# Kernel optimization log

Measured on AMD Instinct MI355X. Metric: run time of the kernel, lower is better.

## Reference

```python
import jax, jax.numpy as jnp
import numpy as np
from jax import lax

NUM_HEADS = 1
DN = ('NCHW', 'OIHW', 'NCHW')
EPS = 1e-12  # F.normalize default eps


def _l2_normalize(t):
    # F.normalize(t, dim=-1): t / max(||t||_2, eps)
    n = jnp.sqrt(jnp.sum(t * t, axis=-1, keepdims=True))
    return t / jnp.maximum(n, EPS)


def setup_inputs() -> dict:
    key = jax.random.key(0)
    k0, k1, k2, k3 = jax.random.split(key, 4)
    b, c, h, w = 4, 48, 256, 256
    x = jax.random.normal(k0, (b, c, h, w), dtype=jnp.float32)
    qkv_w = jax.random.normal(k1, (3 * c, c, 1, 1), dtype=jnp.float32) * 0.05
    dw_w = jax.random.normal(k2, (3 * c, 1, 3, 3), dtype=jnp.float32) * 0.05
    proj_w = jax.random.normal(k3, (c, c, 1, 1), dtype=jnp.float32) * 0.05
    temperature = jnp.ones((NUM_HEADS, 1, 1), dtype=jnp.float32)
    return {"x": x, "qkv_w": qkv_w, "dw_w": dw_w, "proj_w": proj_w,
            "temperature": temperature}


def reference(x, qkv_w, dw_w, proj_w, temperature):
    b, c, h, w = x.shape
    heads = NUM_HEADS
    # 1x1 conv to 3c channels, then 3x3 depthwise conv (groups = 3c)
    qkv = lax.conv_general_dilated(x, qkv_w, (1, 1), 'VALID', dimension_numbers=DN)
    qkv = lax.conv_general_dilated(qkv, dw_w, (1, 1), ((1, 1), (1, 1)),
                                   feature_group_count=3 * c, dimension_numbers=DN)
    q, k, v = jnp.split(qkv, 3, axis=1)
    # [b, heads, c_per_head, h*w]
    q = q.reshape(b, heads, c // heads, h * w)
    k = k.reshape(b, heads, c // heads, h * w)
    v = v.reshape(b, heads, c // heads, h * w)
    q = _l2_normalize(q)
    k = _l2_normalize(k)
    # channel-wise attention: [b, heads, c_per_head, c_per_head]
    attn = jax.nn.softmax(jnp.einsum('bhcn,bhdn->bhcd', q, k) * temperature, axis=-1)
    out = jnp.einsum('bhcd,bhdn->bhcn', attn, v).reshape(b, c, h, w)
    return lax.conv_general_dilated(out, proj_w, (1, 1), 'VALID', dimension_numbers=DN)
```

## Files before the change

### kernel.cpp

```cpp
#include <hip/hip_runtime.h>

#define B 4
#define C 48
#define C3 144
#define H 256
#define W 256
#define HW 65536
#define EPSN 1e-12f

#define TSX 16
#define TSY 12
#define HSX 18
#define HSY 14
#define NTX 16
#define NTY 22
#define NPIX2 192
#define NHALO 252

#define NCHUNK 128
#define CHUNK 512
#define LP 68

#define S_QKV_OFF  ((size_t)0)
#define S_DWQ_OFF  (S_QKV_OFF + (size_t)B * C3 * HW)
#define S_DWK_OFF  (S_DWQ_OFF + (size_t)B * C * HW)
#define S_SP_OFF   (S_DWK_OFF + (size_t)B * C * HW)
#define S_NQP_OFF  (S_SP_OFF + (size_t)B * NCHUNK * C * C)
#define S_NKP_OFF  (S_NQP_OFF + (size_t)B * NCHUNK * C)
#define S_S_OFF    (S_NKP_OFF + (size_t)B * NCHUNK * C)
#define S_NQ_OFF   (S_S_OFF + (size_t)B * C * C)
#define S_NK_OFF   (S_NQ_OFF + (size_t)B * C)
#define S_M_OFF    (S_NK_OFF + (size_t)B * C)
#define S_WT_OFF   (S_M_OFF + (size_t)B * C * C)
#define S_FLOATS   (S_WT_OFF + (size_t)C3 * C)

#define A_DWQ_OFF  ((size_t)0)
#define A_DWK_OFF  (A_DWQ_OFF + (size_t)B * C * HW)
#define A_SP_OFF   (A_DWK_OFF + (size_t)B * C * HW)
#define A_NQP_OFF  (A_SP_OFF + (size_t)B * NCHUNK * C * C)
#define A_NKP_OFF  (A_NQP_OFF + (size_t)B * NCHUNK * C)
#define A_S_OFF    (A_NKP_OFF + (size_t)B * NCHUNK * C)
#define A_NQ_OFF   (A_S_OFF + (size_t)B * C * C)
#define A_NK_OFF   (A_NQ_OFF + (size_t)B * C)
#define A_M_OFF    (A_NK_OFF + (size_t)B * C)
#define A_FLOATS   (A_M_OFF + (size_t)B * C * C)

#define B_S_OFF  0
#define B_NQ_OFF (B * C * C)
#define B_NK_OFF (B_NQ_OFF + B * C)
#define B_M_OFF  (B_NK_OFF + B * C)
#define B_ZERO_N (B * C * C + 2 * B * C)


__global__ __launch_bounds__(256) void s_wt(
    const float* __restrict__ w1, float* __restrict__ wT) {
  const int i = blockIdx.x * 256 + threadIdx.x;
  if (i < C3 * C) {
    const int oc = i / C, d = i - oc * C;
    wT[d * C3 + oc] = w1[i];
  }
}

__global__ __launch_bounds__(256) void s_conv1x1(
    const float* __restrict__ x, const float* __restrict__ wT,
    float* __restrict__ qkv) {
  __shared__ float xs[C * 128];
  const int t = threadIdx.x;
  const int bb = blockIdx.x >> 9;
  const int p0 = (blockIdx.x & 511) << 7;
  const float* xb = x + (size_t)bb * C * HW + p0;
#pragma unroll
  for (int j = 0; j < 6; ++j) {
    const int f = t + j * 256;
    const int d = f >> 5, p4 = (f & 31) * 4;
    *(float4*)&xs[d * 128 + p4] = *(const float4*)&xb[(size_t)d * HW + p4];
  }
  __syncthreads();
  const int pl = (t & 63) * 2;
  const int ocw = __builtin_amdgcn_readfirstlane((t >> 6) * 12);
#pragma unroll 1
  for (int g = 0; g < 3; ++g) {
    const int oc0 = g * 48 + ocw;
    const float* wp = wT + oc0;
    float acc[12][2];
#pragma unroll
    for (int o = 0; o < 12; ++o)
#pragma unroll
      for (int p = 0; p < 2; ++p) acc[o][p] = 0.f;
#pragma unroll 4
    for (int d = 0; d < C; ++d) {
      const float2 xv = *(const float2*)&xs[d * 128 + pl];
      const float xa[2] = {xv.x, xv.y};
#pragma unroll
      for (int jj = 0; jj < 3; ++jj) {
        const float4 wv = *(const float4*)&wp[d * C3 + jj * 4];
        const float wa[4] = {wv.x, wv.y, wv.z, wv.w};
#pragma unroll
        for (int o = 0; o < 4; ++o)
#pragma unroll
          for (int p = 0; p < 2; ++p)
            acc[jj * 4 + o][p] = fmaf(wa[o], xa[p], acc[jj * 4 + o][p]);
      }
    }
    float* ob = qkv + ((size_t)bb * C3 + oc0) * HW + p0 + pl;
#pragma unroll
    for (int o = 0; o < 12; ++o) {
      float2 v;
      v.x = acc[o][0]; v.y = acc[o][1];
      *(float2*)&ob[(size_t)o * HW] = v;
    }
  }
}

#define DWR 16
__global__ __launch_bounds__(256) void s_dw(
    const float* __restrict__ qkv, const float* __restrict__ w9,
    float* __restrict__ dwq, float* __restrict__ dwk,
    float* __restrict__ vout) {
  __shared__ float ls[18 * 260];
  const int t = threadIdx.x;
  const int rblk = blockIdx.x & 15;
  const int cb = blockIdx.x >> 4;
  const int c = cb % C3;
  const int bb = cb / C3;
  const int r0 = rblk * DWR;
  const float* src = qkv + (size_t)cb * HW;
#pragma unroll
  for (int f = t; f < 18 * 256; f += 256) {
    const int rr = f >> 8, xc = f & 255;
    const int gr = r0 - 1 + rr;
    ls[rr * 260 + 1 + xc] = (gr >= 0 && gr < H) ? src[gr * W + xc] : 0.f;
  }
  if (t < 18) { ls[t * 260] = 0.f; ls[t * 260 + 257] = 0.f; }
  const float* wp = w9 + c * 9;
  float wv[9];
#pragma unroll
  for (int k = 0; k < 9; ++k) wv[k] = wp[k];
  __syncthreads();
  float* dst;
  int cc;
  if (c < C)          { dst = dwq;  cc = c; }
  else if (c < 2 * C) { dst = dwk;  cc = c - C; }
  else                { dst = vout; cc = c - 2 * C; }
  float* ob = dst + ((size_t)bb * C + cc) * HW;
  const int xq = (t & 63) * 4;
  const int rw = t >> 6;
#pragma unroll
  for (int rr = rw; rr < DWR; rr += 4) {
    const float* l0 = ls + rr * 260 + xq;
    const float4 a0 = *(const float4*)&l0[0];
    const float2 b0 = *(const float2*)&l0[4];
    const float4 a1 = *(const float4*)&l0[260];
    const float2 b1 = *(const float2*)&l0[264];
    const float4 a2 = *(const float4*)&l0[520];
    const float2 b2 = *(const float2*)&l0[524];
    const float r0e[6] = {a0.x, a0.y, a0.z, a0.w, b0.x, b0.y};
    const float r1e[6] = {a1.x, a1.y, a1.z, a1.w, b1.x, b1.y};
    const float r2e[6] = {a2.x, a2.y, a2.z, a2.w, b2.x, b2.y};
    float4 o;
    float* op = &o.x;
#pragma unroll
    for (int j = 0; j < 4; ++j) {
      float d = wv[0] * r0e[j] + wv[1] * r0e[j + 1] + wv[2] * r0e[j + 2];
      d = fmaf(wv[3], r1e[j], d);
      d = fmaf(wv[4], r1e[j + 1], d);
      d = fmaf(wv[5], r1e[j + 2], d);
      d = fmaf(wv[6], r2e[j], d);
      d = fmaf(wv[7], r2e[j + 1], d);
      d = fmaf(wv[8], r2e[j + 2], d);
      op[j] = d;
    }
    *(float4*)&ob[(r0 + rr) * W + xq] = o;
  }
}


__global__ __launch_bounds__(256) void a1_conv_dw(
    const float* __restrict__ x, const float* __restrict__ w1,
    const float* __restrict__ w9, float* __restrict__ dwq,
    float* __restrict__ dwk, float* __restrict__ vout) {
  __shared__ float xs[C * 256];
  __shared__ float qs[8 * 256];
  __shared__ float wg[C * 8];
  __shared__ float wg9[8 * 9];
  const int t = threadIdx.x;
  const int bb = blockIdx.x / (NTX * NTY);
  const int tile = blockIdx.x % (NTX * NTY);
  const int ty = tile / NTX, tx = tile % NTX;
  const int hyy = t / HSX, hxx = t % HSX;
  const int hy = ty * TSY - 1 + hyy;
  const int hx = tx * TSX - 1 + hxx;
  const bool hin = (t < NHALO) && (hy >= 0) && (hy < H) && (hx >= 0) && (hx < W);
  const float* xb = x + (size_t)bb * C * HW + (hin ? (hy * W + hx) : 0);
#pragma unroll
  for (int ic = 0; ic < C; ++ic)
    xs[ic * 256 + t] = hin ? xb[(size_t)ic * HW] : 0.f;
  const int py = t / TSX, px = t % TSX;
  const int gy = ty * TSY + py, gx = tx * TSX + px;
  const bool pin = (t < NPIX2) && (gy < H);
  const int hpos = py * HSX + px;
  for (int grp = 0; grp < 18; ++grp) {
    const int ch0 = grp * 8;
    {
      const int j = t + ((t < 128) ? 256 : 0);
      if (t < 128) {
        const int ic = t >> 3, g = t & 7;
        wg[t] = w1[(ch0 + g) * C + ic];
        const int ic2 = j >> 3, g2 = j & 7;
        wg[j] = w1[(ch0 + g2) * C + ic2];
      } else if (t < 256) {
        const int r = t - 128;
        const int ic = (r + 128) >> 3, g = (r + 128) & 7;
        wg[r + 128] = w1[(ch0 + g) * C + ic];
      }
      if (t < 72) wg9[t] = w9[ch0 * 9 + t];
    }
    __syncthreads();
    float a[8];
#pragma unroll
    for (int g = 0; g < 8; ++g) a[g] = 0.f;
#pragma unroll 4
    for (int ic = 0; ic < C; ++ic) {
      const float xsv = xs[ic * 256 + t];
      const float4 w0 = *(const float4*)&wg[ic * 8];
      const float4 w4 = *(const float4*)&wg[ic * 8 + 4];
      a[0] = fmaf(w0.x, xsv, a[0]);
      a[1] = fmaf(w0.y, xsv, a[1]);
      a[2] = fmaf(w0.z, xsv, a[2]);
      a[3] = fmaf(w0.w, xsv, a[3]);
      a[4] = fmaf(w4.x, xsv, a[4]);
      a[5] = fmaf(w4.y, xsv, a[5]);
      a[6] = fmaf(w4.z, xsv, a[6]);
      a[7] = fmaf(w4.w, xsv, a[7]);
    }
#pragma unroll
    for (int g = 0; g < 8; ++g) qs[g * 256 + t] = a[g];
    __syncthreads();
    if (t < NPIX2) {
#pragma unroll
      for (int g = 0; g < 8; ++g) {
        const int ch = ch0 + g;
        const float* w9p = wg9 + g * 9;
        const float* q = qs + g * 256 + hpos;
        float d = w9p[0] * q[0] + w9p[1] * q[1] + w9p[2] * q[2];
        d = fmaf(w9p[3], q[HSX], d);
        d = fmaf(w9p[4], q[HSX + 1], d);
        d = fmaf(w9p[5], q[HSX + 2], d);
        d = fmaf(w9p[6], q[2 * HSX], d);
        d = fmaf(w9p[7], q[2 * HSX + 1], d);
        d = fmaf(w9p[8], q[2 * HSX + 2], d);
        if (pin) {
          float* dst;
          int cc;
          if (ch < C)          { dst = dwq; cc = ch; }
          else if (ch < 2 * C) { dst = dwk; cc = ch - C; }
          else                 { dst = vout; cc = ch - 2 * C; }
          dst[((size_t)bb * C + cc) * HW + gy * W + gx] = d;
        }
      }
    }
    __syncthreads();
  }
}

__global__ __launch_bounds__(256) void a2_gram(
    const float* __restrict__ dwq, const float* __restrict__ dwk,
    float* __restrict__ Sp, float* __restrict__ nqp, float* __restrict__ nkp) {
  __shared__ float qs[C * LP];
  __shared__ float ks[C * LP];
  const int tid = threadIdx.x;
  const int bb = blockIdx.x / NCHUNK;
  const int chunk = blockIdx.x % NCHUNK;
  const int base = chunk * CHUNK;
  const float* qb = dwq + (size_t)bb * C * HW + base;
  const float* kb = dwk + (size_t)bb * C * HW + base;
  const int c0 = (tid >> 4) * 3;
  const int d0 = (tid & 15) * 3;
  float acc[3][3] = {{0.f}};
  float nacc = 0.f;
  float4 rq[3], rk[3];
#pragma unroll
  for (int j = 0; j < 3; ++j) {
    const int f = tid + j * 256;
    const int cc = f >> 4, p4 = (f & 15) * 4;
    rq[j] = *(const float4*)&qb[(size_t)cc * HW + p4];
    rk[j] = *(const float4*)&kb[(size_t)cc * HW + p4];
  }
  for (int sub = 0; sub < CHUNK / 64; ++sub) {
    __syncthreads();
#pragma unroll
    for (int j = 0; j < 3; ++j) {
      const int f = tid + j * 256;
      const int cc = f >> 4, p4 = (f & 15) * 4;
      *(float4*)&qs[cc * LP + p4] = rq[j];
      *(float4*)&ks[cc * LP + p4] = rk[j];
    }
    if (sub < CHUNK / 64 - 1) {
#pragma unroll
      for (int j = 0; j < 3; ++j) {
        const int f = tid + j * 256;
        const int cc = f >> 4, p4 = (f & 15) * 4;
        rq[j] = *(const float4*)&qb[(size_t)cc * HW + (sub + 1) * 64 + p4];
        rk[j] = *(const float4*)&kb[(size_t)cc * HW + (sub + 1) * 64 + p4];
      }
    }
    __syncthreads();
    if (tid < C) {
#pragma unroll
      for (int pq = 0; pq < 64; pq += 4) {
        const float4 v = *(const float4*)&qs[tid * LP + pq];
        nacc = fmaf(v.x, v.x, nacc);
        nacc = fmaf(v.y, v.y, nacc);
        nacc = fmaf(v.z, v.z, nacc);
        nacc = fmaf(v.w, v.w, nacc);
      }
    } else if (tid >= 64 && tid < 64 + C) {
      const int cq = tid - 64;
#pragma unroll
      for (int pq = 0; pq < 64; pq += 4) {
        const float4 v = *(const float4*)&ks[cq * LP + pq];
        nacc = fmaf(v.x, v.x, nacc);
        nacc = fmaf(v.y, v.y, nacc);
        nacc = fmaf(v.z, v.z, nacc);
        nacc = fmaf(v.w, v.w, nacc);
      }
    }
#pragma unroll 4
    for (int pq = 0; pq < 64; pq += 4) {
      const float4 q0 = *(const float4*)&qs[(c0 + 0) * LP + pq];
      const float4 q1 = *(const float4*)&qs[(c0 + 1) * LP + pq];
      const float4 q2 = *(const float4*)&qs[(c0 + 2) * LP + pq];
      const float4 k0 = *(const float4*)&ks[(d0 + 0) * LP + pq];
      const float4 k1 = *(const float4*)&ks[(d0 + 1) * LP + pq];
      const float4 k2 = *(const float4*)&ks[(d0 + 2) * LP + pq];
      const float qa[3][4] = {{q0.x, q0.y, q0.z, q0.w},
                              {q1.x, q1.y, q1.z, q1.w},
                              {q2.x, q2.y, q2.z, q2.w}};
      const float ka[3][4] = {{k0.x, k0.y, k0.z, k0.w},
                              {k1.x, k1.y, k1.z, k1.w},
                              {k2.x, k2.y, k2.z, k2.w}};
#pragma unroll
      for (int p = 0; p < 4; ++p)
#pragma unroll
        for (int i = 0; i < 3; ++i)
#pragma unroll
          for (int j = 0; j < 3; ++j)
            acc[i][j] = fmaf(qa[i][p], ka[j][p], acc[i][j]);
    }
  }
  float* Sb = Sp + ((size_t)bb * NCHUNK + chunk) * C * C;
#pragma unroll
  for (int i = 0; i < 3; ++i)
#pragma unroll
    for (int j = 0; j < 3; ++j)
      Sb[(c0 + i) * C + (d0 + j)] = acc[i][j];
  if (tid < C)                        nqp[((size_t)bb * NCHUNK + chunk) * C + tid] = nacc;
  else if (tid >= 64 && tid < 64 + C) nkp[((size_t)bb * NCHUNK + chunk) * C + (tid - 64)] = nacc;
}

#define RED_N (B * C * C + 2 * B * C)
__global__ __launch_bounds__(256) void a3a_reduce(
    const float* __restrict__ Sp, const float* __restrict__ nqp,
    const float* __restrict__ nkp, float* __restrict__ S,
    float* __restrict__ nq, float* __restrict__ nk) {
  const int gid = blockIdx.x * 256 + threadIdx.x;
  if (gid < B * C * C) {
    const int bb = gid / (C * C), j = gid - bb * (C * C);
    const float* src = Sp + (size_t)bb * NCHUNK * C * C + j;
    float s = 0.f;
#pragma unroll 8
    for (int i = 0; i < NCHUNK; ++i) s += src[(size_t)i * C * C];
    S[gid] = s;
  } else if (gid < B * C * C + B * C) {
    const int r = gid - B * C * C;
    const int bb = r / C, j = r - bb * C;
    const float* src = nqp + (size_t)bb * NCHUNK * C + j;
    float s = 0.f;
#pragma unroll 8
    for (int i = 0; i < NCHUNK; ++i) s += src[(size_t)i * C];
    nq[r] = s;
  } else if (gid < RED_N) {
    const int r = gid - B * C * C - B * C;
    const int bb = r / C, j = r - bb * C;
    const float* src = nkp + (size_t)bb * NCHUNK * C + j;
    float s = 0.f;
#pragma unroll 8
    for (int i = 0; i < NCHUNK; ++i) s += src[(size_t)i * C];
    nk[r] = s;
  }
}

__global__ __launch_bounds__(64) void a3b_attn(
    const float* __restrict__ S, const float* __restrict__ nq,
    const float* __restrict__ nk, const float* __restrict__ proj_w,
    const float* __restrict__ temperature, float* __restrict__ MT) {
  __shared__ float A[C * C];
  __shared__ float knl[C];
  const int bb = blockIdx.x;
  const int t = threadIdx.x;
  const float T = temperature[0];
  if (t < C) knl[t] = fmaxf(sqrtf(nk[bb * C + t]), EPSN);
  __syncthreads();
  if (t < C) {
    const float qn = fmaxf(sqrtf(nq[bb * C + t]), EPSN);
    float row[C];
    float m = -1e30f;
    for (int d = 0; d < C; ++d) {
      const float v = S[(size_t)bb * C * C + t * C + d] / (qn * knl[d]) * T;
      row[d] = v;
      m = fmaxf(m, v);
    }
    float sum = 0.f;
    for (int d = 0; d < C; ++d) { const float e = expf(row[d] - m); row[d] = e; sum += e; }
    const float inv = 1.f / sum;
    for (int d = 0; d < C; ++d) A[t * C + d] = row[d] * inv;
  }
  __syncthreads();
  for (int idx = t; idx < C * C; idx += 64) {
    const int e = idx / C, d = idx % C;
    float acc = 0.f;
    for (int cc = 0; cc < C; ++cc) acc = fmaf(proj_w[e * C + cc], A[cc * C + d], acc);
    MT[(size_t)bb * C * C + d * C + e] = acc;
  }
}

__global__ __launch_bounds__(256) void a4_apply(
    float* __restrict__ out, const float* __restrict__ MT) {
  __shared__ float vs[C * 128];
  const int t = threadIdx.x;
  const int bb = blockIdx.x >> 9;
  const int p0 = (blockIdx.x & 511) << 7;
  float* ob = out + (size_t)bb * C * HW + p0;
#pragma unroll
  for (int j = 0; j < 6; ++j) {
    const int f = t + j * 256;
    const int d = f >> 5, p4 = (f & 31) * 4;
    *(float4*)&vs[d * 128 + p4] = *(const float4*)&ob[(size_t)d * HW + p4];
  }
  __syncthreads();
  const int pl = (t & 63) * 2;
  const int e0 = __builtin_amdgcn_readfirstlane((t >> 6) * 12);
  const float* mb = MT + (size_t)bb * C * C + e0;
  float acc[12][2];
#pragma unroll
  for (int o = 0; o < 12; ++o)
#pragma unroll
    for (int p = 0; p < 2; ++p) acc[o][p] = 0.f;
#pragma unroll 4
  for (int d = 0; d < C; ++d) {
    const float2 xv = *(const float2*)&vs[d * 128 + pl];
    const float xa[2] = {xv.x, xv.y};
#pragma unroll
    for (int jj = 0; jj < 3; ++jj) {
      const float4 wv = *(const float4*)&mb[d * C + jj * 4];
      const float wa[4] = {wv.x, wv.y, wv.z, wv.w};
#pragma unroll
      for (int o = 0; o < 4; ++o)
#pragma unroll
        for (int p = 0; p < 2; ++p)
          acc[jj * 4 + o][p] = fmaf(wa[o], xa[p], acc[jj * 4 + o][p]);
    }
  }
#pragma unroll
  for (int o = 0; o < 12; ++o) {
    float2 v;
    v.x = acc[o][0]; v.y = acc[o][1];
    *(float2*)&ob[(size_t)(e0 + o) * HW + pl] = v;
  }
}


__global__ __launch_bounds__(256) void k0_zero(float* __restrict__ ws) {
  const int i = blockIdx.x * 256 + threadIdx.x;
  if (i < B_ZERO_N) ws[i] = 0.f;
}

#define TS 14
#define HS 16
#define NT 19
#define NPIX 196

__global__ __launch_bounds__(256) void k1_fused(
    const float* __restrict__ x, const float* __restrict__ w1,
    const float* __restrict__ w9, float* __restrict__ vout,
    float* __restrict__ S, float* __restrict__ nq, float* __restrict__ nk) {
  __shared__ float qs[4 * 256];
  __shared__ float qt[NPIX * C];
  __shared__ float kt[NPIX * C];
  const int t = threadIdx.x;
  const int bb = blockIdx.x / (NT * NT);
  const int tile = blockIdx.x % (NT * NT);
  const int ty = tile / NT, tx = tile % NT;
  const int hy = ty * TS - 1 + (t >> 4);
  const int hx = tx * TS - 1 + (t & 15);
  const bool hin = (hy >= 0 && hy < H && hx >= 0 && hx < W);
  const float* xb = x + (size_t)bb * C * HW;
  float xv[C];
#pragma unroll
  for (int ic = 0; ic < C; ++ic)
    xv[ic] = hin ? xb[(size_t)ic * HW + hy * W + hx] : 0.f;
  const int py = t / TS, px = t % TS;
  const int gy = ty * TS + py, gx = tx * TS + px;
  const bool pin = (t < NPIX) && (gy < H) && (gx < W);
  for (int grp = 0; grp < 36; ++grp) {
    const int ch0 = grp * 4;
    const float* wp = w1 + ch0 * C;
    float a0 = 0.f, a1 = 0.f, a2 = 0.f, a3 = 0.f;
#pragma unroll
    for (int ic = 0; ic < C; ++ic) {
      const float xs = xv[ic];
      a0 = fmaf(wp[ic], xs, a0);
      a1 = fmaf(wp[C + ic], xs, a1);
      a2 = fmaf(wp[2 * C + ic], xs, a2);
      a3 = fmaf(wp[3 * C + ic], xs, a3);
    }
    qs[0 * 256 + t] = a0;
    qs[1 * 256 + t] = a1;
    qs[2 * 256 + t] = a2;
    qs[3 * 256 + t] = a3;
    __syncthreads();
    if (t < NPIX) {
#pragma unroll
      for (int g = 0; g < 4; ++g) {
        const int ch = ch0 + g;
        const float* w9p = w9 + ch * 9;
        const float* q = qs + g * 256 + py * HS + px;
        float d = w9p[0] * q[0] + w9p[1] * q[1] + w9p[2] * q[2];
        d = fmaf(w9p[3], q[HS], d);
        d = fmaf(w9p[4], q[HS + 1], d);
        d = fmaf(w9p[5], q[HS + 2], d);
        d = fmaf(w9p[6], q[2 * HS], d);
        d = fmaf(w9p[7], q[2 * HS + 1], d);
        d = fmaf(w9p[8], q[2 * HS + 2], d);
        if (ch < C)          qt[t * C + ch] = pin ? d : 0.f;
        else if (ch < 2 * C) kt[t * C + (ch - C)] = pin ? d : 0.f;
        else if (pin)        vout[((size_t)bb * C + (ch - 2 * C)) * HW + gy * W + gx] = d;
      }
    }
    __syncthreads();
  }
  if (t < C) {
    float s = 0.f;
    for (int p = 0; p < NPIX; ++p) { const float v = qt[p * C + t]; s = fmaf(v, v, s); }
    atomicAdd(&nq[bb * C + t], s);
  } else if (t >= 64 && t < 64 + C) {
    const int c = t - 64;
    float s = 0.f;
    for (int p = 0; p < NPIX; ++p) { const float v = kt[p * C + c]; s = fmaf(v, v, s); }
    atomicAdd(&nk[bb * C + c], s);
  }
  {
    const int part = t >> 6;
    const int idx = t & 63;
    const int c0 = (idx >> 3) * 6;
    const int d0 = (idx & 7) * 6;
    float acc[6][6] = {{0.f}};
    const int p0 = part * 49;
    for (int p = p0; p < p0 + 49; ++p) {
      float qv[6], kv[6];
#pragma unroll
      for (int j = 0; j < 6; ++j) { qv[j] = qt[p * C + c0 + j]; kv[j] = kt[p * C + d0 + j]; }
#pragma unroll
      for (int i = 0; i < 6; ++i)
#pragma unroll
        for (int j = 0; j < 6; ++j) acc[i][j] = fmaf(qv[i], kv[j], acc[i][j]);
    }
    float* Sb = S + (size_t)bb * C * C;
#pragma unroll
    for (int i = 0; i < 6; ++i)
#pragma unroll
      for (int j = 0; j < 6; ++j) atomicAdd(&Sb[(c0 + i) * C + (d0 + j)], acc[i][j]);
  }
}


extern "C" void kernel_launch(void* const* d_in, const int* in_sizes, int n_in,
                              void* d_out, int out_size, void* d_ws, size_t ws_size,
                              hipStream_t stream) {
  const float* x      = (const float*)d_in[0];
  const float* qkv_w  = (const float*)d_in[1];
  const float* dw_w   = (const float*)d_in[2];
  const float* proj_w = (const float*)d_in[3];
  const float* temp   = (const float*)d_in[4];
  float* out = (float*)d_out;
  float* ws  = (float*)d_ws;

  if (ws_size >= S_FLOATS * sizeof(float)) {
    float* qkv = ws + S_QKV_OFF;
    float* dwq = ws + S_DWQ_OFF;
    float* dwk = ws + S_DWK_OFF;
    float* Sp  = ws + S_SP_OFF;
    float* nqp = ws + S_NQP_OFF;
    float* nkp = ws + S_NKP_OFF;
    float* S   = ws + S_S_OFF;
    float* nq  = ws + S_NQ_OFF;
    float* nk  = ws + S_NK_OFF;
    float* MT  = ws + S_M_OFF;
    float* wT  = ws + S_WT_OFF;
    s_wt<<<(C3 * C + 255) / 256, 256, 0, stream>>>(qkv_w, wT);
    s_conv1x1<<<B * 512, 256, 0, stream>>>(x, wT, qkv);
    s_dw<<<B * C3 * 16, 256, 0, stream>>>(qkv, dw_w, dwq, dwk, out);
    a2_gram<<<B * NCHUNK, 256, 0, stream>>>(dwq, dwk, Sp, nqp, nkp);
    a3a_reduce<<<(RED_N + 255) / 256, 256, 0, stream>>>(Sp, nqp, nkp, S, nq, nk);
    a3b_attn<<<B, 64, 0, stream>>>(S, nq, nk, proj_w, temp, MT);
    a4_apply<<<B * 512, 256, 0, stream>>>(out, MT);
  } else if (ws_size >= A_FLOATS * sizeof(float)) {
    float* dwq = ws + A_DWQ_OFF;
    float* dwk = ws + A_DWK_OFF;
    float* Sp  = ws + A_SP_OFF;
    float* nqp = ws + A_NQP_OFF;
    float* nkp = ws + A_NKP_OFF;
    float* S   = ws + A_S_OFF;
    float* nq  = ws + A_NQ_OFF;
    float* nk  = ws + A_NK_OFF;
    float* MT  = ws + A_M_OFF;
    a1_conv_dw<<<B * NTX * NTY, 256, 0, stream>>>(x, qkv_w, dw_w, dwq, dwk, out);
    a2_gram<<<B * NCHUNK, 256, 0, stream>>>(dwq, dwk, Sp, nqp, nkp);
    a3a_reduce<<<(RED_N + 255) / 256, 256, 0, stream>>>(Sp, nqp, nkp, S, nq, nk);
    a3b_attn<<<B, 64, 0, stream>>>(S, nq, nk, proj_w, temp, MT);
    a4_apply<<<B * 512, 256, 0, stream>>>(out, MT);
  } else {
    float* S  = ws + B_S_OFF;
    float* nq = ws + B_NQ_OFF;
    float* nk = ws + B_NK_OFF;
    float* MT = ws + B_M_OFF;
    k0_zero<<<(B_ZERO_N + 255) / 256, 256, 0, stream>>>(ws);
    k1_fused<<<B * NT * NT, 256, 0, stream>>>(x, qkv_w, dw_w, out, S, nq, nk);
    a3b_attn<<<B, 64, 0, stream>>>(S, nq, nk, proj_w, temp, MT);
    a4_apply<<<B * 512, 256, 0, stream>>>(out, MT);
  }
}
```

Baseline: 337.8 us.

## Fuse depthwise conv with Gram/norm partials, dropping dwq/dwk intermediates

Replaces the separate depthwise-conv kernel and Gram kernel in the large-workspace path with one kernel per image row. It computes the 3x3 depthwise conv for all 144 channels, keeps q/k in shared memory and accumulates the 48x48 Gram partials and squared norms directly. V is still written out to global memory. This removes the global write and re-read of the dwq/dwk tensors. In exchange, the conv now reads its stencil taps straight from global memory (relying on cache reuse) with one thread per pixel, and there are twice as many partial chunks for the reduce kernel to sum.

```diff
diff --git a/kernel.cpp b/kernel.cpp
--- a/kernel.cpp
+++ b/kernel.cpp
@@ -21,13 +21,14 @@
 #define CHUNK 512
 #define LP 68
 
+#define NCH2 256
+#define LP2 132
+
 #define S_QKV_OFF  ((size_t)0)
-#define S_DWQ_OFF  (S_QKV_OFF + (size_t)B * C3 * HW)
-#define S_DWK_OFF  (S_DWQ_OFF + (size_t)B * C * HW)
-#define S_SP_OFF   (S_DWK_OFF + (size_t)B * C * HW)
-#define S_NQP_OFF  (S_SP_OFF + (size_t)B * NCHUNK * C * C)
-#define S_NKP_OFF  (S_NQP_OFF + (size_t)B * NCHUNK * C)
-#define S_S_OFF    (S_NKP_OFF + (size_t)B * NCHUNK * C)
+#define S_SP_OFF   (S_QKV_OFF + (size_t)B * C3 * HW)
+#define S_NQP_OFF  (S_SP_OFF + (size_t)B * NCH2 * C * C)
+#define S_NKP_OFF  (S_NQP_OFF + (size_t)B * NCH2 * C)
+#define S_S_OFF    (S_NKP_OFF + (size_t)B * NCH2 * C)
 #define S_NQ_OFF   (S_S_OFF + (size_t)B * C * C)
 #define S_NK_OFF   (S_NQ_OFF + (size_t)B * C)
 #define S_M_OFF    (S_NK_OFF + (size_t)B * C)
@@ -112,66 +113,103 @@
   }
 }
 
-#define DWR 16
-__global__ __launch_bounds__(256) void s_dw(
+__global__ __launch_bounds__(256) void s_dwgram(
     const float* __restrict__ qkv, const float* __restrict__ w9,
-    float* __restrict__ dwq, float* __restrict__ dwk,
-    float* __restrict__ vout) {
-  __shared__ float ls[18 * 260];
+    float* __restrict__ vout, float* __restrict__ Sp,
+    float* __restrict__ nqp, float* __restrict__ nkp) {
+  __shared__ float qk[96 * LP2];
   const int t = threadIdx.x;
-  const int rblk = blockIdx.x & 15;
-  const int cb = blockIdx.x >> 4;
-  const int c = cb % C3;
-  const int bb = cb / C3;
-  const int r0 = rblk * DWR;
-  const float* src = qkv + (size_t)cb * HW;
-#pragma unroll
-  for (int f = t; f < 18 * 256; f += 256) {
-    const int rr = f >> 8, xc = f & 255;
-    const int gr = r0 - 1 + rr;
-    ls[rr * 260 + 1 + xc] = (gr >= 0 && gr < H) ? src[gr * W + xc] : 0.f;
-  }
-  if (t < 18) { ls[t * 260] = 0.f; ls[t * 260 + 257] = 0.f; }
-  const float* wp = w9 + c * 9;
-  float wv[9];
-#pragma unroll
-  for (int k = 0; k < 9; ++k) wv[k] = wp[k];
-  __syncthreads();
-  float* dst;
-  int cc;
-  if (c < C)          { dst = dwq;  cc = c; }
-  else if (c < 2 * C) { dst = dwk;  cc = c - C; }
-  else                { dst = vout; cc = c - 2 * C; }
-  float* ob = dst + ((size_t)bb * C + cc) * HW;
-  const int xq = (t & 63) * 4;
-  const int rw = t >> 6;
-#pragma unroll
-  for (int rr = rw; rr < DWR; rr += 4) {
-    const float* l0 = ls + rr * 260 + xq;
-    const float4 a0 = *(const float4*)&l0[0];
-    const float2 b0 = *(const float2*)&l0[4];
-    const float4 a1 = *(const float4*)&l0[260];
-    const float2 b1 = *(const float2*)&l0[264];
-    const float4 a2 = *(const float4*)&l0[520];
-    const float2 b2 = *(const float2*)&l0[524];
-    const float r0e[6] = {a0.x, a0.y, a0.z, a0.w, b0.x, b0.y};
-    const float r1e[6] = {a1.x, a1.y, a1.z, a1.w, b1.x, b1.y};
-    const float r2e[6] = {a2.x, a2.y, a2.z, a2.w, b2.x, b2.y};
-    float4 o;
-    float* op = &o.x;
-#pragma unroll
-    for (int j = 0; j < 4; ++j) {
-      float d = wv[0] * r0e[j] + wv[1] * r0e[j + 1] + wv[2] * r0e[j + 2];
-      d = fmaf(wv[3], r1e[j], d);
-      d = fmaf(wv[4], r1e[j + 1], d);
-      d = fmaf(wv[5], r1e[j + 2], d);
-      d = fmaf(wv[6], r2e[j], d);
-      d = fmaf(wv[7], r2e[j + 1], d);
-      d = fmaf(wv[8], r2e[j + 2], d);
-      op[j] = d;
-    }
-    *(float4*)&ob[(r0 + rr) * W + xq] = o;
-  }
+  const int bb = blockIdx.x >> 8;
+  const int y  = blockIdx.x & 255;
+  const float* qb = qkv + (size_t)bb * C3 * HW;
+  const int lx = t & 127;
+  const int chH = t >> 7;
+  const int c0 = (t >> 4) * 3;
+  const int d0 = (t & 15) * 3;
+  float acc[3][3] = {{0.f}};
+  float nacc = 0.f;
+#pragma unroll 1
+  for (int sub = 0; sub < 2; ++sub) {
+    const int x = sub * 128 + lx;
+    const bool okm = (x > 0);
+    const bool okp = (x < W - 1);
+    __syncthreads();
+#pragma unroll 2
+    for (int cp = 0; cp < 72; ++cp) {
+      const int ch = cp * 2 + chH;
+      const float* wp = w9 + ch * 9;
+      float wv[9];
+#pragma unroll
+      for (int k2 = 0; k2 < 9; ++k2) wv[k2] = wp[k2];
+      float s = 0.f;
+#pragma unroll
+      for (int dy = 0; dy < 3; ++dy) {
+        const int ry = y + dy - 1;
+        if (ry >= 0 && ry < H) {
+          const float* r = qb + (size_t)ch * HW + ry * W;
+          const float vm = okm ? r[x - 1] : 0.f;
+          const float vc = r[x];
+          const float vp = okp ? r[x + 1] : 0.f;
+          s = fmaf(wv[dy * 3 + 0], vm, s);
+          s = fmaf(wv[dy * 3 + 1], vc, s);
+          s = fmaf(wv[dy * 3 + 2], vp, s);
+        }
+      }
+      if (ch < 96) qk[ch * LP2 + lx] = s;
+      else vout[((size_t)bb * C + (ch - 96)) * HW + y * W + x] = s;
+    }
+    __syncthreads();
+    if (t < C) {
+#pragma unroll
+      for (int pq = 0; pq < 128; pq += 4) {
+        const float4 v = *(const float4*)&qk[t * LP2 + pq];
+        nacc = fmaf(v.x, v.x, nacc);
+        nacc = fmaf(v.y, v.y, nacc);
+        nacc = fmaf(v.z, v.z, nacc);
+        nacc = fmaf(v.w, v.w, nacc);
+      }
+    } else if (t >= 64 && t < 64 + C) {
+      const int cq = 48 + (t - 64);
+#pragma unroll
+      for (int pq = 0; pq < 128; pq += 4) {
+        const float4 v = *(const float4*)&qk[cq * LP2 + pq];
+        nacc = fmaf(v.x, v.x, nacc);
+        nacc = fmaf(v.y, v.y, nacc);
+        nacc = fmaf(v.z, v.z, nacc);
+        nacc = fmaf(v.w, v.w, nacc);
+      }
+    }
+#pragma unroll 4
+    for (int pq = 0; pq < 128; pq += 4) {
+      const float4 q0 = *(const float4*)&qk[(c0 + 0) * LP2 + pq];
+      const float4 q1 = *(const float4*)&qk[(c0 + 1) * LP2 + pq];
+      const float4 q2 = *(const float4*)&qk[(c0 + 2) * LP2 + pq];
+      const float4 k0 = *(const float4*)&qk[(48 + d0 + 0) * LP2 + pq];
+      const float4 k1 = *(const float4*)&qk[(48 + d0 + 1) * LP2 + pq];
+      const float4 k2 = *(const float4*)&qk[(48 + d0 + 2) * LP2 + pq];
+      const float qa[3][4] = {{q0.x, q0.y, q0.z, q0.w},
+                              {q1.x, q1.y, q1.z, q1.w},
+                              {q2.x, q2.y, q2.z, q2.w}};
+      const float ka[3][4] = {{k0.x, k0.y, k0.z, k0.w},
+                              {k1.x, k1.y, k1.z, k1.w},
+                              {k2.x, k2.y, k2.z, k2.w}};
+#pragma unroll
+      for (int p = 0; p < 4; ++p)
+#pragma unroll
+        for (int i = 0; i < 3; ++i)
+#pragma unroll
+          for (int j = 0; j < 3; ++j)
+            acc[i][j] = fmaf(qa[i][p], ka[j][p], acc[i][j]);
+    }
+  }
+  float* Sb = Sp + ((size_t)bb * NCH2 + y) * C * C;
+#pragma unroll
+  for (int i = 0; i < 3; ++i)
+#pragma unroll
+    for (int j = 0; j < 3; ++j)
+      Sb[(c0 + i) * C + (d0 + j)] = acc[i][j];
+  if (t < C)                        nqp[((size_t)bb * NCH2 + y) * C + t] = nacc;
+  else if (t >= 64 && t < 64 + C)   nkp[((size_t)bb * NCH2 + y) * C + (t - 64)] = nacc;
 }
 
 
@@ -362,30 +400,30 @@
 __global__ __launch_bounds__(256) void a3a_reduce(
     const float* __restrict__ Sp, const float* __restrict__ nqp,
     const float* __restrict__ nkp, float* __restrict__ S,
-    float* __restrict__ nq, float* __restrict__ nk) {
+    float* __restrict__ nq, float* __restrict__ nk, int nchunk) {
   const int gid = blockIdx.x * 256 + threadIdx.x;
   if (gid < B * C * C) {
     const int bb = gid / (C * C), j = gid - bb * (C * C);
-    const float* src = Sp + (size_t)bb * NCHUNK * C * C + j;
+    const float* src = Sp + (size_t)bb * nchunk * C * C + j;
     float s = 0.f;
 #pragma unroll 8
-    for (int i = 0; i < NCHUNK; ++i) s += src[(size_t)i * C * C];
+    for (int i = 0; i < nchunk; ++i) s += src[(size_t)i * C * C];
     S[gid] = s;
   } else if (gid < B * C * C + B * C) {
     const int r = gid - B * C * C;
     const int bb = r / C, j = r - bb * C;
-    const float* src = nqp + (size_t)bb * NCHUNK * C + j;
+    const float* src = nqp + (size_t)bb * nchunk * C + j;
     float s = 0.f;
 #pragma unroll 8
-    for (int i = 0; i < NCHUNK; ++i) s += src[(size_t)i * C];
+    for (int i = 0; i < nchunk; ++i) s += src[(size_t)i * C];
     nq[r] = s;
   } else if (gid < RED_N) {
     const int r = gid - B * C * C - B * C;
     const int bb = r / C, j = r - bb * C;
-    const float* src = nkp + (size_t)bb * NCHUNK * C + j;
+    const float* src = nkp + (size_t)bb * nchunk * C + j;
     float s = 0.f;
 #pragma unroll 8
-    for (int i = 0; i < NCHUNK; ++i) s += src[(size_t)i * C];
+    for (int i = 0; i < nchunk; ++i) s += src[(size_t)i * C];
     nk[r] = s;
   }
 }
@@ -587,8 +625,6 @@
 
   if (ws_size >= S_FLOATS * sizeof(float)) {
     float* qkv = ws + S_QKV_OFF;
-    float* dwq = ws + S_DWQ_OFF;
-    float* dwk = ws + S_DWK_OFF;
     float* Sp  = ws + S_SP_OFF;
     float* nqp = ws + S_NQP_OFF;
     float* nkp = ws + S_NKP_OFF;
@@ -599,9 +635,8 @@
     float* wT  = ws + S_WT_OFF;
     s_wt<<<(C3 * C + 255) / 256, 256, 0, stream>>>(qkv_w, wT);
     s_conv1x1<<<B * 512, 256, 0, stream>>>(x, wT, qkv);
-    s_dw<<<B * C3 * 16, 256, 0, stream>>>(qkv, dw_w, dwq, dwk, out);
-    a2_gram<<<B * NCHUNK, 256, 0, stream>>>(dwq, dwk, Sp, nqp, nkp);
-    a3a_reduce<<<(RED_N + 255) / 256, 256, 0, stream>>>(Sp, nqp, nkp, S, nq, nk);
+    s_dwgram<<<B * 256, 256, 0, stream>>>(qkv, dw_w, out, Sp, nqp, nkp);
+    a3a_reduce<<<(RED_N + 255) / 256, 256, 0, stream>>>(Sp, nqp, nkp, S, nq, nk, NCH2);
     a3b_attn<<<B, 64, 0, stream>>>(S, nq, nk, proj_w, temp, MT);
     a4_apply<<<B * 512, 256, 0, stream>>>(out, MT);
   } else if (ws_size >= A_FLOATS * sizeof(float)) {
@@ -616,7 +651,7 @@
     float* MT  = ws + A_M_OFF;
     a1_conv_dw<<<B * NTX * NTY, 256, 0, stream>>>(x, qkv_w, dw_w, dwq, dwk, out);
     a2_gram<<<B * NCHUNK, 256, 0, stream>>>(dwq, dwk, Sp, nqp, nkp);
-    a3a_reduce<<<(RED_N + 255) / 256, 256, 0, stream>>>(Sp, nqp, nkp, S, nq, nk);
+    a3a_reduce<<<(RED_N + 255) / 256, 256, 0, stream>>>(Sp, nqp, nkp, S, nq, nk, NCHUNK);
     a3b_attn<<<B, 64, 0, stream>>>(S, nq, nk, proj_w, temp, MT);
     a4_apply<<<B * 512, 256, 0, stream>>>(out, MT);
   } else {
```

New measurement: 537.6 us. +59.2%, slower.
